# Kernel tuning notes

Hardware: AMD Instinct MI355X
Metric: run time of the kernel (lower is better)

## Reference

```python
import jax, jax.numpy as jnp
import numpy as np

SEQLEN, K, OLDK, HEADS = 2048, 1024, 1024, 16
BASE = 10000.0


def rope(x):
    # x: [b, t, K]; RoPENd over 1 channel dim: rotate adjacent pairs
    # pair j at position t rotated by angle t * BASE**(-j/(K/2))
    t = x.shape[1]
    half = K // 2
    theta = 1.0 / (BASE ** (jnp.arange(half, dtype=jnp.float32) / half))  # [half]
    ang = jnp.arange(t, dtype=jnp.float32)[:, None] * theta[None, :]      # [t, half]
    cos, sin = jnp.cos(ang), jnp.sin(ang)
    xr = x.reshape(x.shape[0], t, half, 2)
    xe, xo = xr[..., 0], xr[..., 1]
    re = xe * cos - xo * sin
    im = xe * sin + xo * cos
    return jnp.stack([re, im], axis=-1).reshape(x.shape)


def setup_inputs() -> dict:
    key = jax.random.key(0)
    ks = jax.random.split(key, 5)
    b = 4
    x = jax.random.normal(ks[0], (b, SEQLEN, OLDK), jnp.float32)
    sc_in = 1.0 / np.sqrt(OLDK).astype(np.float32)
    Wq = jax.random.normal(ks[1], (K, OLDK), jnp.float32) * sc_in
    Wk = jax.random.normal(ks[2], (K, OLDK), jnp.float32) * sc_in
    Wv = jax.random.normal(ks[3], (K, OLDK), jnp.float32) * sc_in
    Wu = jax.random.normal(ks[4], (K, K), jnp.float32) * (1.0 / np.sqrt(K).astype(np.float32))
    bu = jnp.zeros((K,), jnp.float32)
    return {"x": x, "Wq": Wq, "Wk": Wk, "Wv": Wv, "Wu": Wu, "bu": bu}


def reference(x, Wq, Wk, Wv, Wu, bu):
    b, t, _ = x.shape
    h = HEADS
    s = K // h  # head dim
    q = rope(x @ Wq.T)   # [b, t, K]
    k = rope(x @ Wk.T)
    v = x @ Wv.T
    # split heads: [b, h, t, s]
    q = q.reshape(b, t, h, s).transpose(0, 2, 1, 3)
    k = k.reshape(b, t, h, s).transpose(0, 2, 1, 3)
    v = v.reshape(b, t, h, s).transpose(0, 2, 1, 3)
    dot = jnp.einsum('bhqd,bhkd->bhqk', q, k) / jnp.sqrt(jnp.float32(s))
    att = jax.nn.softmax(dot, axis=-1)
    out = jnp.einsum('bhqk,bhkd->bhqd', att, v)
    out = out.transpose(0, 2, 1, 3).reshape(b, t, h * s)
    return out @ Wu.T + bu
```

## Files before the change

kernel.cpp:

```cpp
#include <hip/hip_runtime.h>

#define TSEQ 2048
#define KDIM 1024
#define NHEAD 16
#define HDIM 64
#define BATCH 4
#define HALF 512

typedef __attribute__((ext_vector_type(4))) float f32x4;
typedef __attribute__((ext_vector_type(16))) float f32x16;
typedef __attribute__((ext_vector_type(8))) short short8;
typedef __attribute__((ext_vector_type(4))) unsigned short us4;
typedef __attribute__((ext_vector_type(4))) unsigned int u32x4;

#if __has_builtin(__builtin_amdgcn_exp2f)
#define EXP2(x) __builtin_amdgcn_exp2f(x)
#else
#define EXP2(x) __expf((x)*0.6931471805599453f)
#endif

__device__ __forceinline__ unsigned short f2bf(float f){
  unsigned int u = __float_as_uint(f);
  u += 0x7FFFu + ((u >> 16) & 1u);
  return (unsigned short)(u >> 16);
}

__device__ __forceinline__ unsigned int cvtpk(float a, float b){
  unsigned int r;
  asm("v_cvt_pk_bf16_f32 %0, %1, %2" : "=v"(r) : "v"(a), "v"(b));
  return r;
}

__device__ __forceinline__ f32x4 mfma16(short8 a, short8 b, f32x4 c){
  return __builtin_amdgcn_mfma_f32_16x16x32_bf16(a, b, c, 0, 0, 0);
}
__device__ __forceinline__ f32x16 mfma32(short8 a, short8 b, f32x16 c){
  return __builtin_amdgcn_mfma_f32_32x32x16_bf16(a, b, c, 0, 0, 0);
}

__device__ __forceinline__ void gl_lds16(const void* g, void* l){
  __builtin_amdgcn_global_load_lds(
      (const __attribute__((address_space(1))) unsigned int*)g,
      (__attribute__((address_space(3))) unsigned int*)l, 16, 0, 0);
}

__global__ __launch_bounds__(256) void cvt_bf16(const float* __restrict__ in,
                                                unsigned short* __restrict__ out,
                                                int n4){
  int i = blockIdx.x*256 + threadIdx.x;
  if (i >= n4) return;
  f32x4 v = ((const f32x4*)in)[i];
  us4 o;
  o[0] = f2bf(v[0]); o[1] = f2bf(v[1]); o[2] = f2bf(v[2]); o[3] = f2bf(v[3]);
  ((us4*)out)[i] = o;
}

__global__ __launch_bounds__(256) void trig_init(float* __restrict__ cosT,
                                                 float* __restrict__ sinT){
  int idx = blockIdx.x*256 + threadIdx.x;
  int t = idx >> 9;
  int j = idx & (HALF-1);
  float theta = powf(10000.0f, -(float)j * (1.0f/(float)HALF));
  float ang = (float)t * theta;
  cosT[idx] = cosf(ang);
  sinT[idx] = sinf(ang);
}

template<int EPI>
__global__ __launch_bounds__(256) void gemm_bt(
    const unsigned short* __restrict__ A,
    const unsigned short* __restrict__ Bw,
    void* __restrict__ outp,
    const float* __restrict__ cosT,
    const float* __restrict__ sinT,
    const float* __restrict__ bias,
    float scale){
  __shared__ __align__(16) unsigned short As[128*32];
  __shared__ __align__(16) unsigned short Bs[128*32];
  const int t  = threadIdx.x;
  const int tm = blockIdx.x*128, tn = blockIdx.y*128;
  const int w  = t>>6, l = t&63;
  const int wm = (w>>1)*64, wn = (w&1)*64;
  const int lr = l&15, lk = (l>>4)*8, g4 = (l>>4)*4;

  f32x4 acc[4][4];
  #pragma unroll
  for (int i=0;i<4;i++)
    #pragma unroll
    for (int j=0;j<4;j++) acc[i][j] = (f32x4){0.f,0.f,0.f,0.f};

  const int sr = t>>2, sc = (t&3)*8;
  const unsigned short* Ag = A  + (size_t)(tm+sr)*KDIM + sc;
  const unsigned short* Bg = Bw + (size_t)(tn+sr)*KDIM + sc;
  unsigned short* Al0 = As + t*8;
  unsigned short* Al1 = As + 2048 + t*8;
  unsigned short* Bl0 = Bs + t*8;
  unsigned short* Bl1 = Bs + 2048 + t*8;

  for (int k0=0; k0<KDIM; k0+=32){
    gl_lds16(Ag + k0, Al0);
    gl_lds16(Ag + (size_t)64*KDIM + k0, Al1);
    gl_lds16(Bg + k0, Bl0);
    gl_lds16(Bg + (size_t)64*KDIM + k0, Bl1);
    __syncthreads();
    short8 af[4], bfr[4];
    #pragma unroll
    for (int i=0;i<4;i++) af[i]  = *(const short8*)&As[(wm+i*16+lr)*32 + lk];
    #pragma unroll
    for (int j=0;j<4;j++) bfr[j] = *(const short8*)&Bs[(wn+j*16+lr)*32 + lk];
    #pragma unroll
    for (int i=0;i<4;i++)
      #pragma unroll
      for (int j=0;j<4;j++)
        acc[i][j] = mfma16(af[i], bfr[j], acc[i][j]);
    __syncthreads();
  }

  #pragma unroll
  for (int i=0;i<4;i++){
    #pragma unroll
    for (int j=0;j<4;j++){
      #pragma unroll
      for (int r=0;r<4;r++){
        int row = tm + wm + i*16 + g4 + r;
        int col = tn + wn + j*16 + lr;
        float v = acc[i][j][r];
        if constexpr (EPI==0){
          ((unsigned short*)outp)[(size_t)row*KDIM + col] = f2bf(v);
        } else if constexpr (EPI==1){
          float pv = __shfl_xor(v, 1);
          int tp = row & (TSEQ-1);
          int jj = col >> 1;
          float c = cosT[tp*HALF + jj];
          float s = sinT[tp*HALF + jj];
          float res = (col & 1) ? fmaf(pv, s, v*c)
                                : fmaf(v, c, -(pv*s));
          ((unsigned short*)outp)[(size_t)row*KDIM + col] = f2bf(res*scale);
        } else {
          ((float*)outp)[(size_t)row*KDIM + col] = v + bias[col];
        }
      }
    }
  }
}

__global__ __launch_bounds__(256) void karr(const unsigned short* __restrict__ in,
                                            unsigned short* __restrict__ out){
  const int t = threadIdx.x;
  const int tl = blockIdx.x, h = blockIdx.y, b = blockIdx.z;
  const int ks = t>>6, l = t&63, ln = l&31, h2 = l>>5;
  short8 v = *(const short8*)&in[((size_t)b*TSEQ + tl*32 + ln)*KDIM + h*HDIM + ks*16 + h2*8];
  *(short8*)&out[(((size_t)(b*NHEAD + h)*64 + tl)*2048) + t*8] = v;
}

__global__ __launch_bounds__(256) void varr(const unsigned short* __restrict__ in,
                                            unsigned short* __restrict__ out){
  __shared__ __align__(16) unsigned short tile[32][72];
  const int t = threadIdx.x;
  const int tl = blockIdx.x, h = blockIdx.y, b = blockIdx.z;
  const int r = t>>3, c8 = (t&7)*8;
  short8 v = *(const short8*)&in[((size_t)b*TSEQ + tl*32 + r)*KDIM + h*HDIM + c8];
  *(short8*)&tile[r][c8] = v;
  __syncthreads();
  const int dt = t>>7, ks2 = (t>>6)&1;
  const int l = t&63, ln = l&31, h2 = l>>5;
  const int k0 = ks2*16 + h2*8, d = dt*32 + ln;
  unsigned short tmp[8];
  #pragma unroll
  for (int e=0;e<8;e++) tmp[e] = tile[k0+e][d];
  *(short8*)&out[(((size_t)(b*NHEAD + h)*64 + tl)*2048) + t*8] = *(const short8*)tmp;
}

__global__ __launch_bounds__(256, 4) void flash_attn3(
    const unsigned short* __restrict__ Q,
    const unsigned short* __restrict__ Kf,
    const unsigned short* __restrict__ Vf,
    unsigned short* __restrict__ Out){
  __shared__ __align__(16) unsigned short kv[2][4096];
  __shared__ __align__(16) float lbuf[4][32];
  const int t = threadIdx.x;
  const int w = t>>6, l = t&63;
  const int ln = l&31, h = l>>5;
  const int by = blockIdx.y;
  const int b = by>>4, hh = by&15;
  const int q0 = blockIdx.x*128 + w*32;
  const size_t bT = (size_t)b*TSEQ;
  const int hd0 = hh*HDIM;

  short8 qf[4];
  #pragma unroll
  for (int ks=0; ks<4; ks++)
    qf[ks] = *(const short8*)&Q[(bT + q0 + ln)*KDIM + hd0 + ks*16 + h*8];

  const unsigned short* tbK = Kf + (size_t)(b*NHEAD + hh)*64*2048;
  const unsigned short* tbV = Vf + (size_t)(b*NHEAD + hh)*64*2048;

  gl_lds16(tbK + w*512 + l*8, &kv[0][w*512]);
  gl_lds16(tbV + w*512 + l*8, &kv[0][2048 + w*512]);
  __syncthreads();

  f32x16 O0, O1;
  #pragma unroll
  for (int r=0;r<16;r++){ O0[r]=0.f; O1[r]=0.f; }
  float lsum = 0.f;
  int cur = 0;

  for (int tt=0; tt<64; ++tt){
    if (tt < 63){
      gl_lds16(tbK + (size_t)(tt+1)*2048 + w*512 + l*8, &kv[cur^1][w*512]);
      gl_lds16(tbV + (size_t)(tt+1)*2048 + w*512 + l*8, &kv[cur^1][2048 + w*512]);
    }
    short8 kf0 = *(const short8*)&kv[cur][0*512 + l*8];
    short8 kf1 = *(const short8*)&kv[cur][1*512 + l*8];
    short8 kf2 = *(const short8*)&kv[cur][2*512 + l*8];
    short8 kf3 = *(const short8*)&kv[cur][3*512 + l*8];

    f32x16 S;
    #pragma unroll
    for (int r=0;r<16;r++) S[r]=0.f;
    S = mfma32(kf0, qf[0], S);
    S = mfma32(kf1, qf[1], S);
    S = mfma32(kf2, qf[2], S);
    S = mfma32(kf3, qf[3], S);

    float rs = 0.f;
    #pragma unroll
    for (int r=0;r<16;r++){ S[r] = EXP2(S[r]); rs += S[r]; }
    lsum += rs;

    unsigned int wds[8];
    #pragma unroll
    for (int i=0;i<8;i++) wds[i] = cvtpk(S[2*i], S[2*i+1]);

    unsigned int y0 = __shfl_xor(h ? wds[0] : wds[2], 32);
    unsigned int y1 = __shfl_xor(h ? wds[1] : wds[3], 32);
    unsigned int y2 = __shfl_xor(h ? wds[4] : wds[6], 32);
    unsigned int y3 = __shfl_xor(h ? wds[5] : wds[7], 32);

    u32x4 pw0 = h ? (u32x4){y0, y1, wds[2], wds[3]}
                  : (u32x4){wds[0], wds[1], y0, y1};
    u32x4 pw1 = h ? (u32x4){y2, y3, wds[6], wds[7]}
                  : (u32x4){wds[4], wds[5], y2, y3};
    short8 pa0 = *(short8*)&pw0;
    short8 pa1 = *(short8*)&pw1;

    short8 vf;
    vf = *(const short8*)&kv[cur][2048 + 0*512 + l*8];
    O0 = mfma32(pa0, vf, O0);
    vf = *(const short8*)&kv[cur][2048 + 1*512 + l*8];
    O0 = mfma32(pa1, vf, O0);
    vf = *(const short8*)&kv[cur][2048 + 2*512 + l*8];
    O1 = mfma32(pa0, vf, O1);
    vf = *(const short8*)&kv[cur][2048 + 3*512 + l*8];
    O1 = mfma32(pa1, vf, O1);

    __syncthreads();
    cur ^= 1;
  }

  float lfull = lsum + __shfl_xor(lsum, 32);
  float linv = 1.0f / lfull;
  if (h == 0) lbuf[w][ln] = linv;
  __syncthreads();

  #pragma unroll
  for (int g=0; g<4; g++){
    f32x4 lv = *(const f32x4*)&lbuf[w][g*8 + h*4];
    #pragma unroll
    for (int i=0; i<4; i++){
      int r = g*4 + i;
      int row = q0 + g*8 + h*4 + i;
      size_t base = (bT + row)*KDIM + hd0;
      Out[base + ln]      = f2bf(O0[r]*lv[i]);
      Out[base + 32 + ln] = f2bf(O1[r]*lv[i]);
    }
  }
}

extern "C" void kernel_launch(void* const* d_in, const int* in_sizes, int n_in,
                              void* d_out, int out_size, void* d_ws, size_t ws_size,
                              hipStream_t stream){
  (void)in_sizes; (void)n_in; (void)out_size; (void)ws_size;
  const float* x  = (const float*)d_in[0];
  const float* Wq = (const float*)d_in[1];
  const float* Wk = (const float*)d_in[2];
  const float* Wv = (const float*)d_in[3];
  const float* Wu = (const float*)d_in[4];
  const float* bu = (const float*)d_in[5];

  char* ws = (char*)d_ws;
  size_t off = 0;
  auto alloc = [&](size_t bytes){ void* p = ws + off; off += bytes; return p; };
  unsigned short* xb  = (unsigned short*)alloc(16777216);
  unsigned short* qb  = (unsigned short*)alloc(16777216);
  unsigned short* kb  = (unsigned short*)alloc(16777216);
  unsigned short* vb  = (unsigned short*)alloc(16777216);
  unsigned short* kfr = (unsigned short*)alloc(16777216);
  unsigned short* wqb = (unsigned short*)alloc(2097152);
  unsigned short* wkb = (unsigned short*)alloc(2097152);
  unsigned short* wvb = (unsigned short*)alloc(2097152);
  unsigned short* wub = (unsigned short*)alloc(2097152);
  float* cosT = (float*)alloc(4194304);
  float* sinT = (float*)alloc(4194304);
  unsigned short* vfr = kb;
  unsigned short* att = xb;

  cvt_bf16<<<8192, 256, 0, stream>>>(x,  xb,  2097152);
  cvt_bf16<<<1024, 256, 0, stream>>>(Wq, wqb, 262144);
  cvt_bf16<<<1024, 256, 0, stream>>>(Wk, wkb, 262144);
  cvt_bf16<<<1024, 256, 0, stream>>>(Wv, wvb, 262144);
  cvt_bf16<<<1024, 256, 0, stream>>>(Wu, wub, 262144);
  trig_init<<<4096, 256, 0, stream>>>(cosT, sinT);

  dim3 gg(64, 8);
  gemm_bt<1><<<gg, 256, 0, stream>>>(xb, wqb, qb, cosT, sinT, nullptr, 0.18033688011112042f);
  gemm_bt<1><<<gg, 256, 0, stream>>>(xb, wkb, kb, cosT, sinT, nullptr, 1.0f);
  gemm_bt<0><<<gg, 256, 0, stream>>>(xb, wvb, vb, nullptr, nullptr, nullptr, 1.0f);

  karr<<<dim3(64,16,4), 256, 0, stream>>>(kb, kfr);
  varr<<<dim3(64,16,4), 256, 0, stream>>>(vb, vfr);
  flash_attn3<<<dim3(16,64), 256, 0, stream>>>(qb, kfr, vfr, att);
  gemm_bt<2><<<gg, 256, 0, stream>>>(att, wub, d_out, nullptr, nullptr, bu, 1.0f);
}
```

Before: 328.0 us.

## Fuse QKV projections into one swizzled launch and triple-buffer attention K/V loads

The three Q/K/V projection GEMMs are merged into a single launch with a grid of 1536 blocks, and the block index is swizzled so that blocks sharing A rows run together. The flash attention kernel moves from double to triple buffering of K/V tiles, using explicit vmcnt waits and raw barriers so two tiles are in flight at once. It also raises wave priority around the MFMA groups. This is meant to cut launch overhead and tail effects in the projections and to hide global-to-LDS latency in attention. The cost is more LDS per block, which could lower occupancy, and the hand-written waitcnt logic is fragile.

```diff
diff --git a/kernel.cpp b/kernel.cpp
--- a/kernel.cpp
+++ b/kernel.cpp
@@ -66,15 +66,96 @@
   sinT[idx] = sinf(ang);
 }
 
-template<int EPI>
-__global__ __launch_bounds__(256) void gemm_bt(
+__global__ __launch_bounds__(256) void gemm_qkv(
+    const unsigned short* __restrict__ A,
+    const unsigned short* __restrict__ Wq,
+    const unsigned short* __restrict__ Wk,
+    const unsigned short* __restrict__ Wv,
+    unsigned short* __restrict__ Qo,
+    unsigned short* __restrict__ Ko,
+    unsigned short* __restrict__ Vo,
+    const float* __restrict__ cosT,
+    const float* __restrict__ sinT){
+  __shared__ __align__(16) unsigned short As[128*32];
+  __shared__ __align__(16) unsigned short Bs[128*32];
+  const int lin = blockIdx.y*64 + blockIdx.x;
+  const int swz = (lin & 7)*192 + (lin >> 3);
+  const int bx = swz & 63, by = swz >> 6;
+  const int region = by >> 3;
+  const int tm = bx*128, tn = (by & 7)*128;
+  const unsigned short* Bw = region==0 ? Wq : (region==1 ? Wk : Wv);
+  unsigned short* outp     = region==0 ? Qo : (region==1 ? Ko : Vo);
+  const float scale = (region==0) ? 0.18033688011112042f : 1.0f;
+
+  const int t  = threadIdx.x;
+  const int w  = t>>6, l = t&63;
+  const int wm = (w>>1)*64, wn = (w&1)*64;
+  const int lr = l&15, lk = (l>>4)*8, g4 = (l>>4)*4;
+
+  f32x4 acc[4][4];
+  #pragma unroll
+  for (int i=0;i<4;i++)
+    #pragma unroll
+    for (int j=0;j<4;j++) acc[i][j] = (f32x4){0.f,0.f,0.f,0.f};
+
+  const int sr = t>>2, sc = (t&3)*8;
+  const unsigned short* Ag = A  + (size_t)(tm+sr)*KDIM + sc;
+  const unsigned short* Bg = Bw + (size_t)(tn+sr)*KDIM + sc;
+  unsigned short* Al0 = As + t*8;
+  unsigned short* Al1 = As + 2048 + t*8;
+  unsigned short* Bl0 = Bs + t*8;
+  unsigned short* Bl1 = Bs + 2048 + t*8;
+
+  for (int k0=0; k0<KDIM; k0+=32){
+    gl_lds16(Ag + k0, Al0);
+    gl_lds16(Ag + (size_t)64*KDIM + k0, Al1);
+    gl_lds16(Bg + k0, Bl0);
+    gl_lds16(Bg + (size_t)64*KDIM + k0, Bl1);
+    __syncthreads();
+    short8 af[4], bfr[4];
+    #pragma unroll
+    for (int i=0;i<4;i++) af[i]  = *(const short8*)&As[(wm+i*16+lr)*32 + lk];
+    #pragma unroll
+    for (int j=0;j<4;j++) bfr[j] = *(const short8*)&Bs[(wn+j*16+lr)*32 + lk];
+    #pragma unroll
+    for (int i=0;i<4;i++)
+      #pragma unroll
+      for (int j=0;j<4;j++)
+        acc[i][j] = mfma16(af[i], bfr[j], acc[i][j]);
+    __syncthreads();
+  }
+
+  #pragma unroll
+  for (int i=0;i<4;i++){
+    #pragma unroll
+    for (int j=0;j<4;j++){
+      #pragma unroll
+      for (int r=0;r<4;r++){
+        int row = tm + wm + i*16 + g4 + r;
+        int col = tn + wn + j*16 + lr;
+        float v = acc[i][j][r];
+        if (region < 2){
+          float pv = __shfl_xor(v, 1);
+          int tp = row & (TSEQ-1);
+          int jj = col >> 1;
+          float c = cosT[tp*HALF + jj];
+          float s = sinT[tp*HALF + jj];
+          float res = (col & 1) ? fmaf(pv, s, v*c)
+                                : fmaf(v, c, -(pv*s));
+          outp[(size_t)row*KDIM + col] = f2bf(res*scale);
+        } else {
+          outp[(size_t)row*KDIM + col] = f2bf(v);
+        }
+      }
+    }
+  }
+}
+
+__global__ __launch_bounds__(256) void gemm_out(
     const unsigned short* __restrict__ A,
     const unsigned short* __restrict__ Bw,
-    void* __restrict__ outp,
-    const float* __restrict__ cosT,
-    const float* __restrict__ sinT,
-    const float* __restrict__ bias,
-    float scale){
+    float* __restrict__ outp,
+    const float* __restrict__ bias){
   __shared__ __align__(16) unsigned short As[128*32];
   __shared__ __align__(16) unsigned short Bs[128*32];
   const int t  = threadIdx.x;
@@ -124,21 +205,7 @@
       for (int r=0;r<4;r++){
         int row = tm + wm + i*16 + g4 + r;
         int col = tn + wn + j*16 + lr;
-        float v = acc[i][j][r];
-        if constexpr (EPI==0){
-          ((unsigned short*)outp)[(size_t)row*KDIM + col] = f2bf(v);
-        } else if constexpr (EPI==1){
-          float pv = __shfl_xor(v, 1);
-          int tp = row & (TSEQ-1);
-          int jj = col >> 1;
-          float c = cosT[tp*HALF + jj];
-          float s = sinT[tp*HALF + jj];
-          float res = (col & 1) ? fmaf(pv, s, v*c)
-                                : fmaf(v, c, -(pv*s));
-          ((unsigned short*)outp)[(size_t)row*KDIM + col] = f2bf(res*scale);
-        } else {
-          ((float*)outp)[(size_t)row*KDIM + col] = v + bias[col];
-        }
+        outp[(size_t)row*KDIM + col] = acc[i][j][r] + bias[col];
       }
     }
   }
@@ -171,12 +238,12 @@
   *(short8*)&out[(((size_t)(b*NHEAD + h)*64 + tl)*2048) + t*8] = *(const short8*)tmp;
 }
 
-__global__ __launch_bounds__(256, 4) void flash_attn3(
+__global__ __launch_bounds__(256, 4) void flash_attn4(
     const unsigned short* __restrict__ Q,
     const unsigned short* __restrict__ Kf,
     const unsigned short* __restrict__ Vf,
     unsigned short* __restrict__ Out){
-  __shared__ __align__(16) unsigned short kv[2][4096];
+  __shared__ __align__(16) unsigned short kv[3*4096];
   __shared__ __align__(16) float lbuf[4][32];
   const int t = threadIdx.x;
   const int w = t>>6, l = t&63;
@@ -195,33 +262,42 @@
   const unsigned short* tbK = Kf + (size_t)(b*NHEAD + hh)*64*2048;
   const unsigned short* tbV = Vf + (size_t)(b*NHEAD + hh)*64*2048;
 
-  gl_lds16(tbK + w*512 + l*8, &kv[0][w*512]);
-  gl_lds16(tbV + w*512 + l*8, &kv[0][2048 + w*512]);
-  __syncthreads();
+  unsigned short* pA = kv;
+  unsigned short* pB = kv + 4096;
+  unsigned short* pC = kv + 8192;
+
+  auto STG = [&](int tt, unsigned short* buf){
+    gl_lds16(tbK + (size_t)tt*2048 + w*512 + l*8, buf + w*512);
+    gl_lds16(tbV + (size_t)tt*2048 + w*512 + l*8, buf + 2048 + w*512);
+  };
+
+  STG(0, pA);
+  STG(1, pB);
+  asm volatile("s_waitcnt vmcnt(2)" ::: "memory");
+  __builtin_amdgcn_s_barrier();
 
   f32x16 O0, O1;
   #pragma unroll
   for (int r=0;r<16;r++){ O0[r]=0.f; O1[r]=0.f; }
   float lsum = 0.f;
-  int cur = 0;
 
   for (int tt=0; tt<64; ++tt){
-    if (tt < 63){
-      gl_lds16(tbK + (size_t)(tt+1)*2048 + w*512 + l*8, &kv[cur^1][w*512]);
-      gl_lds16(tbV + (size_t)(tt+1)*2048 + w*512 + l*8, &kv[cur^1][2048 + w*512]);
-    }
-    short8 kf0 = *(const short8*)&kv[cur][0*512 + l*8];
-    short8 kf1 = *(const short8*)&kv[cur][1*512 + l*8];
-    short8 kf2 = *(const short8*)&kv[cur][2*512 + l*8];
-    short8 kf3 = *(const short8*)&kv[cur][3*512 + l*8];
+    if (tt < 62) STG(tt+2, pC);
+
+    short8 kf0 = *(const short8*)&pA[0*512 + l*8];
+    short8 kf1 = *(const short8*)&pA[1*512 + l*8];
+    short8 kf2 = *(const short8*)&pA[2*512 + l*8];
+    short8 kf3 = *(const short8*)&pA[3*512 + l*8];
 
     f32x16 S;
     #pragma unroll
     for (int r=0;r<16;r++) S[r]=0.f;
+    __builtin_amdgcn_s_setprio(1);
     S = mfma32(kf0, qf[0], S);
     S = mfma32(kf1, qf[1], S);
     S = mfma32(kf2, qf[2], S);
     S = mfma32(kf3, qf[3], S);
+    __builtin_amdgcn_s_setprio(0);
 
     float rs = 0.f;
     #pragma unroll
@@ -244,18 +320,25 @@
     short8 pa0 = *(short8*)&pw0;
     short8 pa1 = *(short8*)&pw1;
 
-    short8 vf;
-    vf = *(const short8*)&kv[cur][2048 + 0*512 + l*8];
-    O0 = mfma32(pa0, vf, O0);
-    vf = *(const short8*)&kv[cur][2048 + 1*512 + l*8];
-    O0 = mfma32(pa1, vf, O0);
-    vf = *(const short8*)&kv[cur][2048 + 2*512 + l*8];
-    O1 = mfma32(pa0, vf, O1);
-    vf = *(const short8*)&kv[cur][2048 + 3*512 + l*8];
-    O1 = mfma32(pa1, vf, O1);
-
-    __syncthreads();
-    cur ^= 1;
+    short8 vf0 = *(const short8*)&pA[2048 + 0*512 + l*8];
+    short8 vf1 = *(const short8*)&pA[2048 + 1*512 + l*8];
+    short8 vf2 = *(const short8*)&pA[2048 + 2*512 + l*8];
+    short8 vf3 = *(const short8*)&pA[2048 + 3*512 + l*8];
+    __builtin_amdgcn_s_setprio(1);
+    O0 = mfma32(pa0, vf0, O0);
+    O0 = mfma32(pa1, vf1, O0);
+    O1 = mfma32(pa0, vf2, O1);
+    O1 = mfma32(pa1, vf3, O1);
+    __builtin_amdgcn_s_setprio(0);
+
+    if (tt < 62){
+      asm volatile("s_waitcnt vmcnt(2)" ::: "memory");
+    } else {
+      asm volatile("s_waitcnt vmcnt(0)" ::: "memory");
+    }
+    __builtin_amdgcn_s_barrier();
+
+    unsigned short* tp = pA; pA = pB; pB = pC; pC = tp;
   }
 
   float lfull = lsum + __shfl_xor(lsum, 32);
@@ -312,13 +395,11 @@
   cvt_bf16<<<1024, 256, 0, stream>>>(Wu, wub, 262144);
   trig_init<<<4096, 256, 0, stream>>>(cosT, sinT);
 
-  dim3 gg(64, 8);
-  gemm_bt<1><<<gg, 256, 0, stream>>>(xb, wqb, qb, cosT, sinT, nullptr, 0.18033688011112042f);
-  gemm_bt<1><<<gg, 256, 0, stream>>>(xb, wkb, kb, cosT, sinT, nullptr, 1.0f);
-  gemm_bt<0><<<gg, 256, 0, stream>>>(xb, wvb, vb, nullptr, nullptr, nullptr, 1.0f);
+  gemm_qkv<<<dim3(64,24), 256, 0, stream>>>(xb, wqb, wkb, wvb,
+                                            qb, kb, vb, cosT, sinT);
 
   karr<<<dim3(64,16,4), 256, 0, stream>>>(kb, kfr);
   varr<<<dim3(64,16,4), 256, 0, stream>>>(vb, vfr);
-  flash_attn3<<<dim3(16,64), 256, 0, stream>>>(qb, kfr, vfr, att);
-  gemm_bt<2><<<gg, 256, 0, stream>>>(att, wub, d_out, nullptr, nullptr, bu, 1.0f);
-}
+  flash_attn4<<<dim3(16,64), 256, 0, stream>>>(qb, kfr, vfr, att);
+  gemm_out<<<dim3(64,8), 256, 0, stream>>>(att, wub, (float*)d_out, bu);
+}
```

After: 358.9 us. 9.4% more time.
